# Kernel optimization log

Hardware: AMD Instinct MI355X
Metric: run time of the kernel (lower is better)

## Reference

```python
import jax, jax.numpy as jnp
import numpy as np

B, L, D = 4, 8192, 512
H, G = 8, 4
DH = D // H      # head channels = 64
GC = D // G      # group channels = 128
KSZ = 5          # kernel = offset_range_factor
PAD = KSZ // 2   # = 2; applied to BOTH offset convs (second conv has k=1, pad=2 -> length L+4)


def conv1d(x, w, b, pad):
    # x: (N, Cin, L), w: (Cout, Cin, K) torch layout
    y = jax.lax.conv_general_dilated(x, w, (1,), [(pad, pad)],
                                     dimension_numbers=('NCH', 'OIH', 'NCH'))
    return y + b[None, :, None]


def setup_inputs() -> dict:
    key = jax.random.key(0)
    ks = jax.random.split(key, 9)
    s = 0.02
    p = lambda k, shape: jax.random.normal(k, shape, jnp.float32) * s
    return {
        'x': jax.random.normal(ks[0], (B, L, D), jnp.float32),
        'Wq': p(ks[1], (D, D)), 'bq': jnp.zeros((D,), jnp.float32),
        'Wk': p(ks[2], (D, D)), 'bk': jnp.zeros((D,), jnp.float32),
        'Wv': p(ks[3], (D, D)), 'bv': jnp.zeros((D,), jnp.float32),
        'Woff1': p(ks[4], (GC, GC, KSZ)), 'boff1': jnp.zeros((GC,), jnp.float32),
        'Woff2': p(ks[5], (1, GC, 1)), 'boff2': jnp.zeros((1,), jnp.float32),
        'rel_bias': p(ks[6], (1, D, L)),
        'Wout': p(ks[7], (D, D)), 'bout': jnp.zeros((D,), jnp.float32),
    }


def reference(x, Wq, bq, Wk, bk, Wv, bv, Woff1, boff1, Woff2, boff2, rel_bias, Wout, bout):
    Bv, Lv, Dv = x.shape
    xc = jnp.transpose(x, (0, 2, 1))                         # (B, D, L)
    # 1x1 convs == pointwise linear over channels
    q = jnp.einsum('od,bdl->bol', Wq, xc) + bq[None, :, None]
    # offset prediction on grouped queries
    gq = q.reshape(Bv * G, GC, Lv)                            # (BG, GC, L)
    o = conv1d(gq, Woff1, boff1, PAD)                         # (BG, GC, L)
    o = conv1d(o, Woff2, boff2, PAD)                          # (BG, 1, L+4) due to k=1,pad=2
    offset = jnp.tanh(o[:, 0, :]) * KSZ                       # (BG, L+4)
    n = offset.shape[-1]
    vgrid = jnp.arange(n, dtype=x.dtype) + offset             # (BG, L+4)
    g = 2.0 * vgrid / (n - 1) - 1.0                           # normalized to [-1, 1] over n
    # torch grid_sample, align_corners=False, padding_mode='zeros', H = L
    pos = ((g + 1.0) * Lv - 1.0) / 2.0
    p0 = jnp.floor(pos)
    w1 = pos - p0                                             # weight for upper neighbor
    p0i = p0.astype(jnp.int32)
    p1i = p0i + 1
    feats = xc.reshape(Bv * G, GC, Lv)

    def gather(idx):
        valid = ((idx >= 0) & (idx < Lv)).astype(x.dtype)      # (BG, n)
        idxc = jnp.clip(idx, 0, Lv - 1)
        vals = jnp.take_along_axis(feats, idxc[:, None, :].astype(jnp.int32).repeat(1, axis=1), axis=2) if False else jnp.take_along_axis(feats, jnp.broadcast_to(idxc[:, None, :], (Bv * G, GC, n)), axis=2)
        return vals * valid[:, None, :]

    samp = gather(p0i) * (1.0 - w1)[:, None, :] + gather(p1i) * w1[:, None, :]
    x_sampled = samp[:, :, :Lv].reshape(Bv, Dv, Lv)           # (B, D, L)
    k = jnp.einsum('od,bdl->bol', Wk, x_sampled) + bk[None, :, None]
    v = jnp.einsum('od,bdl->bol', Wv, x_sampled) + bv[None, :, None] + rel_bias
    qh = q.reshape(Bv * H, DH, Lv)
    kh = k.reshape(Bv * H, DH, Lv)
    vh = v.reshape(Bv * H, DH, Lv)
    # channel-attention: contraction over sequence length L
    scores = jnp.einsum('bil,bjl->bij', qh, kh) * (Dv ** -0.5)  # (B*H, DH, DH)
    attn = jax.nn.softmax(scores, axis=-1)
    out = jnp.einsum('bij,bjl->bil', attn, vh)                # (B*H, DH, L)
    # rearrange '(b g) l c -> b c (g l)' with b=B, g=H, l=DH, c=L -> (B, L, D)
    out = jnp.transpose(out.reshape(Bv, H, DH, Lv), (0, 3, 1, 2)).reshape(Bv, Lv, H * DH)
    return out @ Wout.T + bout
```

## Files before the change

kernel.cpp:

```cpp
#include <hip/hip_runtime.h>
#include <hip/hip_bf16.h>
#include <math.h>

using u16 = unsigned short;
using u32 = unsigned int;

typedef __attribute__((ext_vector_type(8))) short s16x8;
typedef __attribute__((ext_vector_type(4))) float f32x4;

#define B_  4
#define L_  8192
#define D_  512
#define H_  8
#define G_  4

__device__ __forceinline__ float bf2f(u16 u) {
    u32 x = ((u32)u) << 16;
    return __uint_as_float(x);
}
__device__ __forceinline__ u16 f2bf(float f) {
    u32 x = __float_as_uint(f);
    u32 lsb = (x >> 16) & 1u;
    x += 0x7FFFu + lsb;
    return (u16)(x >> 16);
}
__device__ __forceinline__ void async16(const void* g, void* l) {
    __builtin_amdgcn_global_load_lds((const __attribute__((address_space(1))) u32*)g,
                                     (__attribute__((address_space(3))) u32*)l, 16, 0, 0);
}
#define WAIT_VM16  0x4F70
#define WAIT_VM8   0x0F78
#define WAIT_VM0   0x0F70
#define WAIT_LGKM0 0xC07F

#define CAST_BLOCKS 16384
#define PACK_BLOCKS 384
__global__ __launch_bounds__(256) void prep_kernel(const float* __restrict__ x,
                                                   u16* __restrict__ x_bf,
                                                   const float* __restrict__ Wq,
                                                   const float* __restrict__ Wk,
                                                   const float* __restrict__ Wv,
                                                   u16* __restrict__ Pq,
                                                   u16* __restrict__ Pk,
                                                   u16* __restrict__ Pv,
                                                   const float* __restrict__ W1,
                                                   const float* __restrict__ b1,
                                                   const float* __restrict__ W2,
                                                   const float* __restrict__ b2,
                                                   float* __restrict__ weff) {
    const int bid = blockIdx.x;
    const int tid = threadIdx.x;
    if (bid < CAST_BLOCKS) {
        const int i = bid * 256 + tid;
        float4 v = ((const float4*)x)[i];
        ushort4 o;
        o.x = f2bf(v.x); o.y = f2bf(v.y); o.z = f2bf(v.z); o.w = f2bf(v.w);
        ((ushort4*)x_bf)[i] = o;
    } else if (bid < CAST_BLOCKS + PACK_BLOCKS) {
        const int pb = bid - CAST_BLOCKS;
        const int wsel = pb >> 7;
        const int xb = pb & 127;
        const int g = xb * 4 + (tid >> 6);
        const int lane = tid & 63;
        const int cb = g >> 4, kc = g & 15;
        const int q = lane >> 4, fm = lane & 15;
        const float* W = (wsel == 0) ? Wq : (wsel == 1) ? Wk : Wv;
        u16* P = (wsel == 0) ? Pq : (wsel == 1) ? Pk : Pv;
        const float* src = W + (size_t)(cb * 16 + fm) * 512 + kc * 32 + q * 8;
        float4 a = *(const float4*)src;
        float4 b = *(const float4*)(src + 4);
        ushort4 o0, o1;
        o0.x = f2bf(a.x); o0.y = f2bf(a.y); o0.z = f2bf(a.z); o0.w = f2bf(a.w);
        o1.x = f2bf(b.x); o1.y = f2bf(b.y); o1.z = f2bf(b.z); o1.w = f2bf(b.w);
        u16* dst = P + (size_t)g * 512 + lane * 8;
        *(ushort4*)dst = o0;
        *(ushort4*)(dst + 4) = o1;
    } else {
        const int idx = (bid - CAST_BLOCKS - PACK_BLOCKS) * 256 + tid;
        if (idx < 640) {
            int cin = idx / 5, dk = idx % 5;
            float acc = 0.f;
            for (int c = 0; c < 128; ++c) acc += W2[c] * W1[(c * 128 + cin) * 5 + dk];
            weff[idx] = acc;
        } else if (idx == 640) {
            float s = b2[0];
            for (int c = 0; c < 128; ++c) s += W2[c] * b1[c];
            weff[640] = s;
        } else if (idx == 641) {
            weff[641] = b2[0];
        }
    }
}

__global__ __launch_bounds__(256) void offsets_kernel(const u16* __restrict__ qT,
                                                      const float* __restrict__ weff,
                                                      int* __restrict__ p0o,
                                                      float* __restrict__ w1o) {
    __shared__ u16 qs[128 * 72];
    __shared__ float wf[642];
    __shared__ float red[4][64];
    const int tid = threadIdx.x;
    const int t0 = blockIdx.x * 64;
    const int bg = blockIdx.y;
    const int b = bg >> 2, g = bg & 3;
    for (int i = tid; i < 642; i += 256) wf[i] = weff[i];
    for (int i = tid; i < 128 * 9; i += 256) {
        const int ch = i / 9, seg = i - ch * 9;
        const int l = t0 - 8 + seg * 8;
        s16x8 val = {0, 0, 0, 0, 0, 0, 0, 0};
        if (l >= 0)
            val = *(const s16x8*)(qT + (size_t)(b * D_ + g * 128 + ch) * L_ + l);
        *(s16x8*)(qs + ch * 72 + seg * 8) = val;
    }
    __syncthreads();
    const int w = tid >> 6, lane = tid & 63;
    float acc = 0.f;
    for (int c = 0; c < 32; ++c) {
        const int ch = w * 32 + c;
        const u16* row = qs + ch * 72 + lane + 4;
        const float* wr = wf + ch * 5;
        #pragma unroll
        for (int dk = 0; dk < 5; ++dk) acc += wr[dk] * bf2f(row[dk]);
    }
    red[w][lane] = acc;
    __syncthreads();
    if (w == 0) {
        const float s = red[0][lane] + red[1][lane] + red[2][lane] + red[3][lane];
        const int t = t0 + lane;
        const float o2 = (t >= 2) ? (s + wf[640]) : wf[641];
        const double offv = tanh((double)o2) * 5.0;
        const double vg  = (double)t + offv;
        const double gg  = 2.0 * vg / 8195.0 - 1.0;
        const double pos = ((gg + 1.0) * 8192.0 - 1.0) * 0.5;
        const double p0d = floor(pos);
        p0o[(size_t)bg * L_ + t] = (int)p0d;
        w1o[(size_t)bg * L_ + t] = (float)(pos - p0d);
    }
}

__global__ __launch_bounds__(256) void sample_bf16(const u16* __restrict__ xb,
                                                   const int* __restrict__ p0i,
                                                   const float* __restrict__ w1f,
                                                   u16* __restrict__ xs) {
    const size_t idx = (size_t)blockIdx.x * 256 + threadIdx.x;
    const int d8 = (int)(idx & 63);
    const int t = (int)((idx >> 6) & 8191);
    const int b = (int)(idx >> 19);
    const int g = d8 >> 4;
    const size_t og = (size_t)(b * 4 + g) * L_ + t;
    const int p0 = p0i[og];
    const float w1 = w1f[og];
    const float w0 = 1.f - w1;
    const int p1 = p0 + 1;
    s16x8 a = {0, 0, 0, 0, 0, 0, 0, 0}, c = {0, 0, 0, 0, 0, 0, 0, 0};
    if (p0 >= 0 && p0 < L_) a = *(const s16x8*)(xb + ((size_t)b * L_ + p0) * D_ + d8 * 8);
    if (p1 >= 0 && p1 < L_) c = *(const s16x8*)(xb + ((size_t)b * L_ + p1) * D_ + d8 * 8);
    u16 o[8];
    #pragma unroll
    for (int j = 0; j < 8; ++j)
        o[j] = f2bf(bf2f(((const u16*)&a)[j]) * w0 + bf2f(((const u16*)&c)[j]) * w1);
    *(s16x8*)(xs + idx * 8) = *(const s16x8*)o;
}

__global__ __launch_bounds__(256) void sample_f32(const float* __restrict__ x,
                                                  const int* __restrict__ p0i,
                                                  const float* __restrict__ w1f,
                                                  u16* __restrict__ xs) {
    const size_t idx4 = (size_t)blockIdx.x * 256 + threadIdx.x;
    const int d4 = (int)(idx4 & 127);
    const int t = (int)((idx4 >> 7) & 8191);
    const int b = (int)(idx4 >> 20);
    const int g = d4 >> 5;
    const size_t og = (size_t)(b * 4 + g) * L_ + t;
    const int p0 = p0i[og];
    const float w1 = w1f[og];
    const float w0 = 1.f - w1;
    const int p1 = p0 + 1;
    float4 v0 = {0.f, 0.f, 0.f, 0.f}, v1 = {0.f, 0.f, 0.f, 0.f};
    if (p0 >= 0 && p0 < L_) v0 = *(const float4*)(x + ((size_t)b * L_ + p0) * D_ + d4 * 4);
    if (p1 >= 0 && p1 < L_) v1 = *(const float4*)(x + ((size_t)b * L_ + p1) * D_ + d4 * 4);
    ushort4 o;
    o.x = f2bf(v0.x * w0 + v1.x * w1);
    o.y = f2bf(v0.y * w0 + v1.y * w1);
    o.z = f2bf(v0.z * w0 + v1.z * w1);
    o.w = f2bf(v0.w * w0 + v1.w * w1);
    ((ushort4*)xs)[idx4] = o;
}

template <int MODE>
__global__ __launch_bounds__(256) void gemm_kernel(const u16* __restrict__ A,
                                                   const u16* __restrict__ P0,
                                                   const u16* __restrict__ P1,
                                                   const float* __restrict__ bias0,
                                                   const float* __restrict__ bias1,
                                                   const float* __restrict__ rel,
                                                   void* __restrict__ out0,
                                                   void* __restrict__ out1) {
    __shared__ short lds[4][3][2048];
    const int tid = threadIdx.x;
    const int wave = tid >> 6, lane = tid & 63;
    const int bid = blockIdx.x;
    const int xcd = bid & 7;
    const int kk_ = bid >> 3;
    int r0, c0, sel;
    if (MODE == 1) { r0 = (xcd * 32 + (kk_ >> 3)) * 128; sel = (kk_ >> 2) & 1; c0 = (kk_ & 3) * 128; }
    else           { r0 = (xcd * 32 + (kk_ >> 2)) * 128; sel = 0;              c0 = (kk_ & 3) * 128; }
    const u16* P = (MODE == 1 && sel) ? P1 : P0;
    if (MODE == 2) P += (size_t)(r0 >> 13) * 262144;
    const float* bias = (MODE == 1 && sel) ? bias1 : bias0;
    void* out = (MODE == 1 && sel) ? out1 : out0;

    const int wm = (wave >> 1) * 64, wn = (wave & 1) * 64;
    const int srow = lane >> 2;
    const int scol = ((lane & 3) ^ ((srow >> 1) & 3)) * 8;
    const u16* gA = A + (size_t)(r0 + wm) * D_ + scol;
    short* bufA[3] = { &lds[wave][0][0], &lds[wave][1][0], &lds[wave][2][0] };
    const int cbase = (c0 + wn) >> 4;

    f32x4 acc[4][4];
    #pragma unroll
    for (int mi = 0; mi < 4; ++mi)
        #pragma unroll
        for (int ni = 0; ni < 4; ++ni) acc[mi][ni] = (f32x4){0.f, 0.f, 0.f, 0.f};

    const int fm = lane & 15;
    const int sblk = ((lane >> 4) ^ ((fm >> 1) & 3)) * 8;

    s16x8 bfrag[3][4];

    auto issueA = [&](int slot, int it) {
        const int k0 = it * 32;
        #pragma unroll
        for (int j = 0; j < 4; ++j)
            async16(gA + (size_t)(j * 16 + srow) * D_ + k0, bufA[slot] + j * 512);
    };
    auto issueB = [&](int slot, int it) {
        #pragma unroll
        for (int ni = 0; ni < 4; ++ni)
            bfrag[slot][ni] = *(const s16x8*)(P + ((size_t)((cbase + ni) * 16 + it) * 64 + lane) * 8);
    };

    issueA(0, 0); issueB(0, 0);
    issueA(1, 1); issueB(1, 1);
    issueA(2, 2); issueB(2, 2);

    #pragma unroll
    for (int it = 0; it < 16; ++it) {
        const int slot = it % 3;
        if (it < 14)       __builtin_amdgcn_s_waitcnt(WAIT_VM16);
        else if (it == 14) __builtin_amdgcn_s_waitcnt(WAIT_VM8);
        else               __builtin_amdgcn_s_waitcnt(WAIT_VM0);
        __builtin_amdgcn_sched_barrier(0);
        s16x8 af[4];
        #pragma unroll
        for (int mi = 0; mi < 4; ++mi)
            af[mi] = *(const s16x8*)(bufA[slot] + mi * 512 + fm * 32 + sblk);
        __builtin_amdgcn_s_waitcnt(WAIT_LGKM0);
        __builtin_amdgcn_sched_barrier(0);
        if (it < 13) issueA(slot, it + 3);
        #pragma unroll
        for (int mi = 0; mi < 4; ++mi)
            #pragma unroll
            for (int ni = 0; ni < 4; ++ni)
                acc[mi][ni] = __builtin_amdgcn_mfma_f32_16x16x32_bf16(af[mi], bfrag[slot][ni], acc[mi][ni], 0, 0, 0);
        if (it < 13) issueB(slot, it + 3);
    }

    const int fn = lane & 15;
    const int q4 = (lane >> 4) * 4;
    const bool transposed = (MODE == 0) || (MODE == 1 && sel == 0);
    #pragma unroll
    for (int mi = 0; mi < 4; ++mi) {
        #pragma unroll
        for (int ni = 0; ni < 4; ++ni) {
            const int c = c0 + wn + ni * 16 + fn;
            const float bsum = bias[c];
            if (MODE == 2) {
                #pragma unroll
                for (int rg = 0; rg < 4; ++rg) {
                    const int r = r0 + wm + mi * 16 + q4 + rg;
                    ((float*)out)[(size_t)r * D_ + c] = acc[mi][ni][rg] + bsum;
                }
            } else if (transposed) {
                const int r_ = r0 + wm + mi * 16 + q4;
                const int bb = r_ >> 13;
                const int l  = r_ & (L_ - 1);
                ushort4 o;
                o.x = f2bf(acc[mi][ni][0] + bsum);
                o.y = f2bf(acc[mi][ni][1] + bsum);
                o.z = f2bf(acc[mi][ni][2] + bsum);
                o.w = f2bf(acc[mi][ni][3] + bsum);
                *(ushort4*)((u16*)out + (size_t)(bb * D_ + c) * L_ + l) = o;
            } else {
                const int r_ = r0 + wm + mi * 16 + q4;
                const int l  = r_ & (L_ - 1);
                const float4 rl = *(const float4*)(rel + (size_t)c * L_ + l);
                ((u16*)out)[(size_t)(r_ + 0) * D_ + c] = f2bf(acc[mi][ni][0] + bsum + rl.x);
                ((u16*)out)[(size_t)(r_ + 1) * D_ + c] = f2bf(acc[mi][ni][1] + bsum + rl.y);
                ((u16*)out)[(size_t)(r_ + 2) * D_ + c] = f2bf(acc[mi][ni][2] + bsum + rl.z);
                ((u16*)out)[(size_t)(r_ + 3) * D_ + c] = f2bf(acc[mi][ni][3] + bsum + rl.w);
            }
        }
    }
}

__global__ __launch_bounds__(256) void scores_partial(const u16* __restrict__ qT,
                                                      const u16* __restrict__ kT,
                                                      float* __restrict__ part) {
    __shared__ u16 qs[64 * 136];
    __shared__ u16 ks[64 * 136];
    const int chunk = blockIdx.x;
    const int bh = blockIdx.y;
    const int b = bh >> 3, h = bh & 7;
    const int tid = threadIdx.x;
    const int wave = tid >> 6, lane = tid & 63;
    const int wr = (wave >> 1) * 32;
    const int wc = (wave & 1) * 32;
    f32x4 acc[2][2];
    #pragma unroll
    for (int mi = 0; mi < 2; ++mi)
        #pragma unroll
        for (int ni = 0; ni < 2; ++ni) acc[mi][ni] = (f32x4){0.f, 0.f, 0.f, 0.f};
    const size_t base = (size_t)(b * D_ + h * 64) * L_;
    const int m = lane & 15, q = lane >> 4;
    for (int iter = 0; iter < 4; ++iter) {
        const int l0 = chunk * 512 + iter * 128;
        __syncthreads();
        for (int i = tid; i < 1024; i += 256) {
            const int lb = i & 15, ch = i >> 4;
            const size_t gidx = base + (size_t)ch * L_ + l0 + lb * 8;
            *(s16x8*)(qs + ch * 136 + lb * 8) = *(const s16x8*)(qT + gidx);
            *(s16x8*)(ks + ch * 136 + lb * 8) = *(const s16x8*)(kT + gidx);
        }
        __syncthreads();
        #pragma unroll
        for (int kst = 0; kst < 4; ++kst) {
            const int kk = kst * 32 + q * 8;
            s16x8 af[2], bfr[2];
            af[0]  = *(const s16x8*)(qs + (wr + m) * 136 + kk);
            af[1]  = *(const s16x8*)(qs + (wr + 16 + m) * 136 + kk);
            bfr[0] = *(const s16x8*)(ks + (wc + m) * 136 + kk);
            bfr[1] = *(const s16x8*)(ks + (wc + 16 + m) * 136 + kk);
            #pragma unroll
            for (int mi = 0; mi < 2; ++mi)
                #pragma unroll
                for (int ni = 0; ni < 2; ++ni)
                    acc[mi][ni] = __builtin_amdgcn_mfma_f32_16x16x32_bf16(af[mi], bfr[ni], acc[mi][ni], 0, 0, 0);
        }
    }
    float* dst = part + (size_t)(bh * 16 + chunk) * 4096;
    const int q4 = (lane >> 4) * 4;
    #pragma unroll
    for (int mi = 0; mi < 2; ++mi) {
        #pragma unroll
        for (int ni = 0; ni < 2; ++ni) {
            const int j = wc + ni * 16 + m;
            #pragma unroll
            for (int rg = 0; rg < 4; ++rg) {
                const int i = wr + mi * 16 + q4 + rg;
                dst[i * 64 + j] = acc[mi][ni][rg];
            }
        }
    }
}

__global__ __launch_bounds__(256) void softmax_kernel(const float* __restrict__ part,
                                                      float* __restrict__ attn) {
    const int tid = threadIdx.x;
    const int wave = tid >> 6, lane = tid & 63;
    const int row = blockIdx.x * 4 + wave;
    const int bh = row >> 6, i = row & 63;
    float s = 0.f;
    #pragma unroll
    for (int c = 0; c < 16; ++c) s += part[((size_t)(bh * 16 + c)) * 4096 + i * 64 + lane];
    s *= 0.04419417382415922f;
    float m = s;
    for (int off = 32; off > 0; off >>= 1) m = fmaxf(m, __shfl_xor(m, off));
    float e = expf(s - m);
    float sum = e;
    for (int off = 32; off > 0; off >>= 1) sum += __shfl_xor(sum, off);
    attn[(size_t)bh * 4096 + i * 64 + lane] = e / sum;
}

__global__ __launch_bounds__(256) void build_M(const float* __restrict__ Wout,
                                               const float* __restrict__ attn,
                                               u16* __restrict__ Mpack) {
    const int idx = blockIdx.x * 256 + threadIdx.x;
    const int col = idx & 511;
    const int o = (idx >> 9) & 511;
    const int b = idx >> 18;
    const int h = col >> 6, j0 = col & 63;
    const float* wr = Wout + o * 512 + h * 64;
    const float* ar = attn + (size_t)(b * H_ + h) * 4096 + j0;
    float s = 0.f;
    #pragma unroll 8
    for (int i = 0; i < 64; ++i) s += wr[i] * ar[i * 64];
    const int cb = o >> 4, fm = o & 15;
    const int kc = col >> 5, q = (col >> 3) & 3, j = col & 7;
    Mpack[(size_t)b * 262144 + ((size_t)(cb * 16 + kc) * 64 + q * 16 + fm) * 8 + j] = f2bf(s);
}

extern "C" void kernel_launch(void* const* d_in, const int* in_sizes, int n_in,
                              void* d_out, int out_size, void* d_ws, size_t ws_size,
                              hipStream_t stream) {
    const float* x    = (const float*)d_in[0];
    const float* Wq   = (const float*)d_in[1];
    const float* bq   = (const float*)d_in[2];
    const float* Wk   = (const float*)d_in[3];
    const float* bk   = (const float*)d_in[4];
    const float* Wv   = (const float*)d_in[5];
    const float* bv   = (const float*)d_in[6];
    const float* Wo1  = (const float*)d_in[7];
    const float* bo1  = (const float*)d_in[8];
    const float* Wo2  = (const float*)d_in[9];
    const float* bo2  = (const float*)d_in[10];
    const float* rel  = (const float*)d_in[11];
    const float* Wout = (const float*)d_in[12];
    const float* bout = (const float*)d_in[13];

    char* ws = (char*)d_ws;
    const size_t MB = 1024ull * 1024ull;
    const bool big = ws_size >= 165ull * MB;

    u16* x_bf = (u16*)(ws);
    u16* qT   = (u16*)(ws + 32 * MB);
    u16* kT   = (u16*)(ws + 64 * MB);
    u16* v_bf = (u16*)(ws + 96 * MB);

    u16*   xs;
    u16*   Pq; u16* Pk; u16* Pv;
    float* weff; int* p0i; float* w1f;
    float* part; float* attn; u16* Mpack;

    if (big) {
        xs    = (u16*)(ws + 128 * MB);
        part  = (float*)(ws + 128 * MB);
        attn  = (float*)((char*)part + 8 * MB);
        Mpack = (u16*)((char*)attn + 524288);
        Pq    = (u16*)(ws + 160 * MB);
        Pk    = Pq + 262144;
        Pv    = Pk + 262144;
        weff  = (float*)(ws + 162 * MB);
        p0i   = (int*)(ws + 162 * MB + 65536);
        w1f   = (float*)((char*)p0i + 524288);
    } else {
        xs    = x_bf;
        Pq    = (u16*)(ws + 128 * MB);
        Pk    = Pq + 262144;
        Pv    = Pk + 262144;
        weff  = (float*)(ws + 130 * MB);
        p0i   = (int*)(ws + 130 * MB + 65536);
        w1f   = (float*)((char*)p0i + 524288);
        part  = (float*)((char*)w1f + 524288);
        attn  = (float*)((char*)part + 8 * MB);
        Mpack = (u16*)((char*)attn + 524288);
    }

    prep_kernel<<<CAST_BLOCKS + PACK_BLOCKS + 3, 256, 0, stream>>>(
        x, x_bf, Wq, Wk, Wv, Pq, Pk, Pv, Wo1, bo1, Wo2, bo2, weff);
    gemm_kernel<0><<<1024, 256, 0, stream>>>(x_bf, Pq, nullptr, bq, nullptr, nullptr, (void*)qT, nullptr);
    offsets_kernel<<<dim3(128, 16), 256, 0, stream>>>(qT, weff, p0i, w1f);
    if (big) sample_bf16<<<8192, 256, 0, stream>>>(x_bf, p0i, w1f, xs);
    else     sample_f32<<<16384, 256, 0, stream>>>(x, p0i, w1f, xs);
    gemm_kernel<1><<<2048, 256, 0, stream>>>(xs, Pk, Pv, bk, bv, rel, (void*)kT, (void*)v_bf);
    scores_partial<<<dim3(16, 32), 256, 0, stream>>>(qT, kT, part);
    softmax_kernel<<<512, 256, 0, stream>>>(part, attn);
    build_M<<<4096, 256, 0, stream>>>(Wout, attn, Mpack);
    gemm_kernel<2><<<1024, 256, 0, stream>>>(v_bf, Mpack, nullptr, bout, nullptr, nullptr, d_out, nullptr);
}
```

Measured before the change: 384.8 us.

## Share A tile across waves with block-wide double-buffered LDS and barriers

Replaces the per-wave triple-buffered A staging with a block-shared 128x32 A tile that is double-buffered and synchronized with __syncthreads each k-step. Each wave now loads only 32 rows of A instead of 64, which removes duplicate global loads of A between waves that share rows. B fragments are loaded just in time rather than prefetched three steps ahead. This trades deeper prefetch and explicit waitcnt scheduling for less LDS and fewer A loads, but adds a barrier per iteration and shortens the latency hiding.

```diff
diff --git a/kernel.cpp b/kernel.cpp
--- a/kernel.cpp
+++ b/kernel.cpp
@@ -28,10 +28,6 @@
     __builtin_amdgcn_global_load_lds((const __attribute__((address_space(1))) u32*)g,
                                      (__attribute__((address_space(3))) u32*)l, 16, 0, 0);
 }
-#define WAIT_VM16  0x4F70
-#define WAIT_VM8   0x0F78
-#define WAIT_VM0   0x0F70
-#define WAIT_LGKM0 0xC07F
 
 #define CAST_BLOCKS 16384
 #define PACK_BLOCKS 384
@@ -196,7 +192,7 @@
                                                    const float* __restrict__ rel,
                                                    void* __restrict__ out0,
                                                    void* __restrict__ out1) {
-    __shared__ short lds[4][3][2048];
+    __shared__ __align__(16) short abuf[2][128 * 32];
     const int tid = threadIdx.x;
     const int wave = tid >> 6, lane = tid & 63;
     const int bid = blockIdx.x;
@@ -213,8 +209,7 @@
     const int wm = (wave >> 1) * 64, wn = (wave & 1) * 64;
     const int srow = lane >> 2;
     const int scol = ((lane & 3) ^ ((srow >> 1) & 3)) * 8;
-    const u16* gA = A + (size_t)(r0 + wm) * D_ + scol;
-    short* bufA[3] = { &lds[wave][0][0], &lds[wave][1][0], &lds[wave][2][0] };
+    const u16* gA = A + (size_t)(r0 + wave * 32) * D_ + scol;
     const int cbase = (c0 + wn) >> 4;
 
     f32x4 acc[4][4];
@@ -226,44 +221,39 @@
     const int fm = lane & 15;
     const int sblk = ((lane >> 4) ^ ((fm >> 1) & 3)) * 8;
 
-    s16x8 bfrag[3][4];
-
-    auto issueA = [&](int slot, int it) {
+    s16x8 bfrag[4];
+
+    auto stageA = [&](int bsel, int it) {
         const int k0 = it * 32;
         #pragma unroll
-        for (int j = 0; j < 4; ++j)
-            async16(gA + (size_t)(j * 16 + srow) * D_ + k0, bufA[slot] + j * 512);
+        for (int j = 0; j < 2; ++j)
+            async16(gA + (size_t)(j * 16 + srow) * D_ + k0,
+                    &abuf[bsel][wave * 1024 + j * 512]);
     };
-    auto issueB = [&](int slot, int it) {
+    auto loadB = [&](int it) {
         #pragma unroll
         for (int ni = 0; ni < 4; ++ni)
-            bfrag[slot][ni] = *(const s16x8*)(P + ((size_t)((cbase + ni) * 16 + it) * 64 + lane) * 8);
+            bfrag[ni] = *(const s16x8*)(P + ((size_t)((cbase + ni) * 16 + it) * 64 + lane) * 8);
     };
 
-    issueA(0, 0); issueB(0, 0);
-    issueA(1, 1); issueB(1, 1);
-    issueA(2, 2); issueB(2, 2);
+    stageA(0, 0);
+    __syncthreads();
 
     #pragma unroll
     for (int it = 0; it < 16; ++it) {
-        const int slot = it % 3;
-        if (it < 14)       __builtin_amdgcn_s_waitcnt(WAIT_VM16);
-        else if (it == 14) __builtin_amdgcn_s_waitcnt(WAIT_VM8);
-        else               __builtin_amdgcn_s_waitcnt(WAIT_VM0);
-        __builtin_amdgcn_sched_barrier(0);
+        const int cur = it & 1;
+        loadB(it);
+        if (it < 15) stageA(cur ^ 1, it + 1);
         s16x8 af[4];
         #pragma unroll
         for (int mi = 0; mi < 4; ++mi)
-            af[mi] = *(const s16x8*)(bufA[slot] + mi * 512 + fm * 32 + sblk);
-        __builtin_amdgcn_s_waitcnt(WAIT_LGKM0);
-        __builtin_amdgcn_sched_barrier(0);
-        if (it < 13) issueA(slot, it + 3);
+            af[mi] = *(const s16x8*)(&abuf[cur][(wm + mi * 16 + fm) * 32 + sblk]);
         #pragma unroll
         for (int mi = 0; mi < 4; ++mi)
             #pragma unroll
             for (int ni = 0; ni < 4; ++ni)
-                acc[mi][ni] = __builtin_amdgcn_mfma_f32_16x16x32_bf16(af[mi], bfrag[slot][ni], acc[mi][ni], 0, 0, 0);
-        if (it < 13) issueB(slot, it + 3);
+                acc[mi][ni] = __builtin_amdgcn_mfma_f32_16x16x32_bf16(af[mi], bfrag[ni], acc[mi][ni], 0, 0, 0);
+        __syncthreads();
     }
 
     const int fn = lane & 15;
```

Result: no change. 382.1 us (-0.7%).
